# Kernel tuning notes

Hardware: AMD Instinct MI355X
Metric: run time of the kernel (lower is better)

## Reference

```python
import jax, jax.numpy as jnp
import numpy as np

NUM_NODES = 50000
NUM_EDGES = 800000
INPUT_DIM = 256
OUTPUT_DIM = 256
NUM_HEADS = 8
HEAD_DIM = OUTPUT_DIM // NUM_HEADS


def setup_inputs() -> dict:
    key = jax.random.key(0)
    ks = jax.random.split(key, 14)
    x = jax.random.normal(ks[0], (NUM_NODES, INPUT_DIM), dtype=jnp.float32)
    edge_index = jax.random.randint(ks[1], (2, NUM_EDGES), 0, NUM_NODES, dtype=jnp.int32)
    # timestamps in seconds over ~11.5 days so log1p(|dt|/3600) is informative
    edge_time = jax.random.uniform(ks[2], (NUM_EDGES,), dtype=jnp.float32) * 1e6
    node_time = jax.random.uniform(ks[3], (NUM_NODES,), dtype=jnp.float32) * 1e6
    s_in = 1.0 / np.sqrt(INPUT_DIM)
    s_out = 1.0 / np.sqrt(OUTPUT_DIM)
    s_t = 1.0 / np.sqrt(2.0)
    Wq = jax.random.uniform(ks[4], (INPUT_DIM, OUTPUT_DIM), jnp.float32, -s_in, s_in)
    bq = jax.random.uniform(ks[5], (OUTPUT_DIM,), jnp.float32, -s_in, s_in)
    Wk = jax.random.uniform(ks[6], (INPUT_DIM, OUTPUT_DIM), jnp.float32, -s_in, s_in)
    bk = jax.random.uniform(ks[7], (OUTPUT_DIM,), jnp.float32, -s_in, s_in)
    Wv = jax.random.uniform(ks[8], (INPUT_DIM, OUTPUT_DIM), jnp.float32, -s_in, s_in)
    bv = jax.random.uniform(ks[9], (OUTPUT_DIM,), jnp.float32, -s_in, s_in)
    Wt = jax.random.uniform(ks[10], (2, NUM_HEADS), jnp.float32, -s_t, s_t)
    bt = jax.random.uniform(ks[11], (NUM_HEADS,), jnp.float32, -s_t, s_t)
    Wo = jax.random.uniform(ks[12], (OUTPUT_DIM, OUTPUT_DIM), jnp.float32, -s_out, s_out)
    bo = jax.random.uniform(ks[13], (OUTPUT_DIM,), jnp.float32, -s_out, s_out)
    return {"x": x, "edge_index": edge_index, "edge_time": edge_time, "node_time": node_time,
            "Wq": Wq, "bq": bq, "Wk": Wk, "bk": bk, "Wv": Wv, "bv": bv,
            "Wt": Wt, "bt": bt, "Wo": Wo, "bo": bo}


def reference(x, edge_index, edge_time, node_time, Wq, bq, Wk, bk, Wv, bv, Wt, bt, Wo, bo):
    n = x.shape[0]
    q = (x @ Wq + bq).reshape(n, NUM_HEADS, HEAD_DIM)
    k = (x @ Wk + bk).reshape(n, NUM_HEADS, HEAD_DIM)
    v = (x @ Wv + bv).reshape(n, NUM_HEADS, HEAD_DIM)
    src, dst = edge_index[0], edge_index[1]
    # temporal features per edge
    time_diff = edge_time - node_time[dst]
    time_features = jnp.stack(
        [jnp.sign(time_diff), jnp.log1p(jnp.abs(time_diff) / 3600.0)], axis=-1)  # [E, 2]
    temporal_weights = time_features @ Wt + bt  # [E, H]
    scale = HEAD_DIM ** -0.5
    scores = jnp.einsum('ehd,ehd->eh', q[dst], k[src]) * scale + temporal_weights  # [E, H]
    # softmax over ALL edges per head (dim=0), as in the original
    alpha = jax.nn.softmax(scores, axis=0)  # [E, H]
    msg = alpha[..., None] * v[src]  # [E, H, D]
    out = jax.ops.segment_sum(msg, dst, num_segments=n)  # [N, H, D]
    out = out.reshape(n, OUTPUT_DIM)
    return out @ Wo + bo
```

## Files before the change

kernel.cpp:

```cpp
#include <hip/hip_runtime.h>
#include <hip/hip_bf16.h>

#define NUM_NODES 50000
#define NUM_EDGES 800000
#define NUM_HEADS 8
#define HEAD_DIM 32
#define SCAN_BLOCKS 49
#define NCHUNK32 1563

typedef unsigned short ushort8 __attribute__((ext_vector_type(8)));
typedef float f32x4 __attribute__((ext_vector_type(4)));
typedef __bf16 bf16x8 __attribute__((ext_vector_type(8)));
typedef _Float16 h2 __attribute__((ext_vector_type(2)));

union BF8 { ushort8 u; bf16x8 b; };
union H8 { ushort8 u; h2 h[4]; };

#if defined(__has_builtin)
#if __has_builtin(__builtin_amdgcn_fdot2)
#define FDOT2(a, b, c) __builtin_amdgcn_fdot2((a), (b), (c), false)
#endif
#endif
#ifndef FDOT2
#define FDOT2(a, b, c) ((float)(a)[0] * (float)(b)[0] + (float)(a)[1] * (float)(b)[1] + (c))
#endif

__device__ __forceinline__ float bf2f(unsigned short u) {
    return __uint_as_float(((unsigned)u) << 16);
}
__device__ __forceinline__ unsigned short f2bf(float f) {
    unsigned u = __float_as_uint(f);
    unsigned r = (u + 0x7fffu + ((u >> 16) & 1u)) >> 16;
    return (unsigned short)r;
}
__device__ __forceinline__ unsigned short f2h(float f) {
    _Float16 h = (_Float16)f;
    return *(unsigned short*)&h;
}
__device__ __forceinline__ float h2f(unsigned short u) {
    _Float16 h = *(const _Float16*)&u;
    return (float)h;
}

__global__ __launch_bounds__(256) void deg_kernel(const int* __restrict__ dst_idx, int* __restrict__ deg) {
    int e = blockIdx.x * 256 + threadIdx.x;
    if (e < NUM_EDGES) atomicAdd(&deg[dst_idx[e]], 1);
}

__global__ __launch_bounds__(1024) void scanA_kernel(
    const int* __restrict__ deg, int* __restrict__ offs, int* __restrict__ blocksum)
{
    __shared__ int buf[1024];
    int tid = threadIdx.x;
    int i = blockIdx.x * 1024 + tid;
    int v = (i < NUM_NODES) ? deg[i] : 0;
    buf[tid] = v;
    __syncthreads();
    for (int off = 1; off < 1024; off <<= 1) {
        int t = (tid >= off) ? buf[tid - off] : 0;
        __syncthreads();
        buf[tid] += t;
        __syncthreads();
    }
    if (i < NUM_NODES) offs[i] = buf[tid] - v;
    if (tid == 1023) blocksum[blockIdx.x] = buf[1023];
}

__global__ __launch_bounds__(64) void scanB_kernel(
    const int* __restrict__ blocksum, int* __restrict__ carry, int* __restrict__ offs)
{
    if (threadIdx.x == 0) {
        int acc = 0;
        for (int b = 0; b < SCAN_BLOCKS; b++) { carry[b] = acc; acc += blocksum[b]; }
        offs[NUM_NODES] = acc;
    }
}

__global__ __launch_bounds__(256) void scanC_kernel(
    int* __restrict__ offs, const int* __restrict__ carry, int* __restrict__ cursor)
{
    int i = blockIdx.x * 256 + threadIdx.x;
    if (i < NUM_NODES) {
        int v = offs[i] + carry[i >> 10];
        offs[i] = v;
        cursor[i] = v;
    }
}

__global__ __launch_bounds__(256) void fillA_kernel(
    const int* __restrict__ dst_idx, int* __restrict__ cursor, int* __restrict__ edge_of)
{
    int e = blockIdx.x * 256 + threadIdx.x;
    if (e < NUM_EDGES) {
        int pos = atomicAdd(&cursor[dst_idx[e]], 1);
        edge_of[pos] = e;
    }
}

__global__ __launch_bounds__(256) void fillB_kernel(
    const int* __restrict__ edge_of,
    const int* __restrict__ src_idx, const int* __restrict__ dst_idx,
    const float* __restrict__ edge_time, const float* __restrict__ node_time,
    unsigned long long* __restrict__ edata)
{
    int pos = blockIdx.x * 256 + threadIdx.x;
    if (pos < NUM_EDGES) {
        int e = __builtin_nontemporal_load(&edge_of[pos]);
        int s = src_idx[e];
        int d = dst_idx[e];
        float td = edge_time[e] - node_time[d];
        float t0 = (td > 0.f) ? 1.f : ((td < 0.f) ? -1.f : 0.f);
        float t1 = log1pf(fabsf(td) * (1.f / 3600.f));
        unsigned lo = (unsigned)s | ((unsigned)d << 16);
        unsigned hi = (unsigned)f2h(t0) | ((unsigned)f2h(t1) << 16);
        unsigned long long v = (unsigned long long)lo | ((unsigned long long)hi << 32);
        __builtin_nontemporal_store(v, &edata[pos]);
    }
}

__global__ __launch_bounds__(256) void wtrans_kernel(
    const float* __restrict__ Wq, const float* __restrict__ Wk,
    const float* __restrict__ Wv, const float* __restrict__ Wo,
    unsigned short* __restrict__ Wt)
{
    __shared__ float t[64][65];
    int nb = blockIdx.x * 64;
    int kb = blockIdx.y * 64;
    int g = nb >> 8;
    const float* W = (g == 0) ? Wq : (g == 1) ? Wk : (g == 2) ? Wv : Wo;
    int n0 = nb & 255;
    int tx = threadIdx.x & 63;
    int ty = threadIdx.x >> 6;
#pragma unroll
    for (int i = 0; i < 16; i++) {
        int k = i * 4 + ty;
        t[tx][k] = W[(size_t)(kb + k) * 256 + n0 + tx];
    }
    __syncthreads();
#pragma unroll
    for (int i = 0; i < 16; i++) {
        int n = i * 4 + ty;
        Wt[(size_t)(nb + n) * 256 + kb + tx] = f2bf(t[n][tx]);
    }
}

__global__ __launch_bounds__(256) void wpack_kernel(
    const unsigned short* __restrict__ Wt, unsigned short* __restrict__ Wpk)
{
    int gid = blockIdx.x * 256 + threadIdx.x;
    int lane = gid & 63;
    int fragidx = gid >> 6;
    int c2 = fragidx & 7;
    int nf = (fragidx >> 3) & 3;
    int cb = (fragidx >> 5) & 3;
    int g = fragidx >> 7;
    int l16 = lane & 15;
    int kg = lane >> 4;
    int n_col = g * 256 + cb * 64 + nf * 16 + l16;
    int k0 = c2 * 32 + kg * 8;
    ushort8 v = *(const ushort8*)(Wt + (size_t)n_col * 256 + k0);
    *(ushort8*)(Wpk + (size_t)gid * 8) = v;
}

__global__ __launch_bounds__(256) void gemm_qkv_mfma7(
    const float* __restrict__ A, int M,
    const unsigned short* __restrict__ Wpk,
    const float* __restrict__ b0, const float* __restrict__ b1, const float* __restrict__ b2,
    unsigned short* __restrict__ O0, unsigned short* __restrict__ O1, unsigned short* __restrict__ O2)
{
    __shared__ unsigned short As[64 * 256];
    int tid = threadIdx.x;
    int rowbase = blockIdx.x * 64;

    {
        int rsub = tid >> 6;
        int c4 = (tid & 63) * 4;
        int cchunk = (tid & 63) >> 1;
        int sub = (tid & 1);
#pragma unroll
        for (int it = 0; it < 16; it++) {
            int row = it * 4 + rsub;
            int grow = rowbase + row;
            float4 av = make_float4(0.f, 0.f, 0.f, 0.f);
            if (grow < M) av = *(const float4*)(A + (size_t)grow * 256 + c4);
            ushort4 o;
            o.x = f2bf(av.x); o.y = f2bf(av.y); o.z = f2bf(av.z); o.w = f2bf(av.w);
            unsigned byte = row * 512 + ((unsigned)(cchunk ^ (row & 7)) << 4) + sub * 8;
            *(ushort4*)((char*)As + byte) = o;
        }
    }
    __syncthreads();

    int lane = tid & 63;
    int wid = tid >> 6;
    int l16 = lane & 15;
    int kg = lane >> 4;

#pragma unroll
    for (int p = 0; p < 3; p++) {
        const float* bias = (p == 0) ? b0 : (p == 1) ? b1 : b2;
        unsigned short* O = (p == 0) ? O0 : (p == 1) ? O1 : O2;

        f32x4 acc[4][4];
#pragma unroll
        for (int m = 0; m < 4; m++)
#pragma unroll
            for (int n = 0; n < 4; n++) acc[m][n] = (f32x4)(0.0f);

        const ushort8* wbase = (const ushort8*)(Wpk + ((size_t)(p * 4 + wid) * 2048 + lane) * 8);

#pragma unroll
        for (int c2 = 0; c2 < 8; c2++) {
            bf16x8 wfr[4];
#pragma unroll
            for (int n = 0; n < 4; n++) {
                BF8 t; t.u = wbase[(n * 8 + c2) * 64];
                wfr[n] = t.b;
            }
            bf16x8 afr[4];
#pragma unroll
            for (int m = 0; m < 4; m++) {
                int row = m * 16 + l16;
                int cchunk = (c2 * 4 + kg) ^ (row & 7);
                BF8 t;
                t.u = *(const ushort8*)((const char*)As + row * 512 + (cchunk << 4));
                afr[m] = t.b;
            }
#pragma unroll
            for (int m = 0; m < 4; m++)
#pragma unroll
                for (int n = 0; n < 4; n++)
                    acc[m][n] = __builtin_amdgcn_mfma_f32_16x16x32_bf16(wfr[n], afr[m], acc[m][n], 0, 0, 0);
        }

#pragma unroll
        for (int m = 0; m < 4; m++) {
            int node = rowbase + m * 16 + l16;
            if (node >= M) continue;
#pragma unroll
            for (int n = 0; n < 4; n++) {
                int lc = wid * 64 + n * 16 + kg * 4;
                float4 bv = *(const float4*)(bias + lc);
                ushort4 o;
                if (p < 2) {
                    o.x = f2h(acc[m][n][0] + bv.x);
                    o.y = f2h(acc[m][n][1] + bv.y);
                    o.z = f2h(acc[m][n][2] + bv.z);
                    o.w = f2h(acc[m][n][3] + bv.w);
                } else {
                    o.x = f2bf(acc[m][n][0] + bv.x);
                    o.y = f2bf(acc[m][n][1] + bv.y);
                    o.z = f2bf(acc[m][n][2] + bv.z);
                    o.w = f2bf(acc[m][n][3] + bv.w);
                }
                int hh = lc >> 5, dd = lc & 31;
                *(ushort4*)(O + ((size_t)hh * NUM_NODES + node) * 32 + dd) = o;
            }
        }
    }
}

__global__ __launch_bounds__(256) void gemm_out_mfma6(
    const unsigned short* __restrict__ aggb, int M,
    const unsigned short* __restrict__ Wpk,
    const float* __restrict__ bias, const float* __restrict__ kscale,
    float* __restrict__ C)
{
    __shared__ unsigned short As[64 * 256];
    int tid = threadIdx.x;
    int rowbase = blockIdx.x * 64;

    {
        int rsub = tid >> 6;
        int c4 = (tid & 63) * 4;
        int cchunk = (tid & 63) >> 1;
        int sub = (tid & 1);
        int hh = c4 >> 5, dd = c4 & 31;
        float ks = kscale[hh];
#pragma unroll
        for (int it = 0; it < 16; it++) {
            int row = it * 4 + rsub;
            int grow = rowbase + row;
            ushort4 av = make_ushort4(0, 0, 0, 0);
            if (grow < M) av = *(const ushort4*)(aggb + ((size_t)hh * NUM_NODES + grow) * 32 + dd);
            ushort4 o;
            o.x = f2bf(bf2f(av.x) * ks); o.y = f2bf(bf2f(av.y) * ks);
            o.z = f2bf(bf2f(av.z) * ks); o.w = f2bf(bf2f(av.w) * ks);
            unsigned byte = row * 512 + ((unsigned)(cchunk ^ (row & 7)) << 4) + sub * 8;
            *(ushort4*)((char*)As + byte) = o;
        }
    }
    __syncthreads();

    int lane = tid & 63;
    int wid = tid >> 6;
    int l16 = lane & 15;
    int kg = lane >> 4;

    f32x4 acc[4][4];
#pragma unroll
    for (int m = 0; m < 4; m++)
#pragma unroll
        for (int n = 0; n < 4; n++) acc[m][n] = (f32x4)(0.0f);

    const ushort8* wbase = (const ushort8*)(Wpk + ((size_t)wid * 2048 + lane) * 8);

#pragma unroll
    for (int c2 = 0; c2 < 8; c2++) {
        bf16x8 wfr[4];
#pragma unroll
        for (int n = 0; n < 4; n++) {
            BF8 t; t.u = wbase[(n * 8 + c2) * 64];
            wfr[n] = t.b;
        }
        bf16x8 afr[4];
#pragma unroll
        for (int m = 0; m < 4; m++) {
            int row = m * 16 + l16;
            int cchunk = (c2 * 4 + kg) ^ (row & 7);
            BF8 t;
            t.u = *(const ushort8*)((const char*)As + row * 512 + (cchunk << 4));
            afr[m] = t.b;
        }
#pragma unroll
        for (int m = 0; m < 4; m++)
#pragma unroll
            for (int n = 0; n < 4; n++)
                acc[m][n] = __builtin_amdgcn_mfma_f32_16x16x32_bf16(wfr[n], afr[m], acc[m][n], 0, 0, 0);
    }

#pragma unroll
    for (int m = 0; m < 4; m++) {
        int node = rowbase + m * 16 + l16;
        if (node >= M) continue;
#pragma unroll
        for (int n = 0; n < 4; n++) {
            int col = wid * 64 + n * 16 + kg * 4;
            float4 bv = *(const float4*)(bias + col);
            float4 o;
            o.x = acc[m][n][0] + bv.x;
            o.y = acc[m][n][1] + bv.y;
            o.z = acc[m][n][2] + bv.z;
            o.w = acc[m][n][3] + bv.w;
            *(float4*)(C + (size_t)node * 256 + col) = o;
        }
    }
}

__global__ __launch_bounds__(256) void edge_fused_kernel(
    const unsigned short* __restrict__ qh, const unsigned short* __restrict__ kh,
    const unsigned short* __restrict__ vh, const unsigned long long* __restrict__ edata,
    const int* __restrict__ offs, const float* __restrict__ Wt,
    const float* __restrict__ bt, unsigned short* __restrict__ aggb,
    float* __restrict__ psum_part)
{
    __shared__ int sSrc[512];
    __shared__ float sP[512];
    __shared__ float blocksum;
    int tid = threadIdx.x;
    int h = blockIdx.x & 7;
    int chunk = blockIdx.x >> 3;
    int nodebase = chunk * 32;
    float wt0 = Wt[h], wt1 = Wt[8 + h], btv = bt[h];
    const unsigned short* qhh = qh + (size_t)h * NUM_NODES * 32;
    const unsigned short* khh = kh + (size_t)h * NUM_NODES * 32;
    const unsigned short* vhh = vh + (size_t)h * NUM_NODES * 32;
    if (tid == 0) blocksum = 0.f;

    int gg = tid >> 3;
    int j = (tid >> 2) & 1;
    int ln4 = tid & 3;
    int node = nodebase + gg;

    int blkstart = offs[nodebase];
    int nb_hi = (nodebase + 32 < NUM_NODES) ? (nodebase + 32) : NUM_NODES;
    int blkend = offs[nb_hi];
    int start = 0, end = 0;
    if (node < NUM_NODES) { start = offs[node]; end = offs[node + 1]; }

    f32x4 a0 = (f32x4)(0.f), a1 = (f32x4)(0.f);
    float ps = 0.f;

    for (int t0 = blkstart; t0 < blkend; t0 += 512) {
        int cnt = min(512, blkend - t0);
        __syncthreads();
        for (int i = tid; i < cnt; i += 256) {
            unsigned long long ed = __builtin_nontemporal_load(&edata[t0 + i]);
            unsigned lo32 = (unsigned)(ed & 0xffffffffull);
            unsigned hi32 = (unsigned)(ed >> 32);
            int s = lo32 & 0xffffu;
            int d = lo32 >> 16;
            float tf0 = h2f((unsigned short)(hi32 & 0xffffu));
            float tf1 = h2f((unsigned short)(hi32 >> 16));
            const ushort8* kp = (const ushort8*)(khh + (size_t)s * 32);
            const ushort8* qp = (const ushort8*)(qhh + (size_t)d * 32);
            float dotv = 0.f;
#pragma unroll
            for (int u = 0; u < 4; u++) {
                H8 a, b;
                a.u = qp[u]; b.u = kp[u];
#pragma unroll
                for (int jj = 0; jj < 4; jj++) dotv = FDOT2(a.h[jj], b.h[jj], dotv);
            }
            float sc = dotv * 0.17677669529663687f + (tf0 * wt0 + tf1 * wt1 + btv);
            sc = fminf(sc, 80.f);
            float p = __expf(sc);
            sSrc[i] = s;
            sP[i] = p;
            ps += p;
        }
        __syncthreads();
        int lo = (start > t0) ? start : t0;
        int hi = (end < t0 + cnt) ? end : (t0 + cnt);
        for (int cb = lo + j; cb < hi; cb += 2) {
            int i0 = cb - t0;
            int s0 = sSrc[i0];
            float p0 = sP[i0];
            ushort8 v = *(const ushort8*)(vhh + (size_t)s0 * 32 + ln4 * 8);
            a0[0] += p0 * bf2f(v[0]); a0[1] += p0 * bf2f(v[1]);
            a0[2] += p0 * bf2f(v[2]); a0[3] += p0 * bf2f(v[3]);
            a1[0] += p0 * bf2f(v[4]); a1[1] += p0 * bf2f(v[5]);
            a1[2] += p0 * bf2f(v[6]); a1[3] += p0 * bf2f(v[7]);
        }
    }

#pragma unroll
    for (int i = 0; i < 4; i++) {
        a0[i] += __shfl_xor(a0[i], 4, 64);
        a1[i] += __shfl_xor(a1[i], 4, 64);
    }
    if (node < NUM_NODES && j == 0) {
        ushort8 o;
        o[0] = f2bf(a0[0]); o[1] = f2bf(a0[1]); o[2] = f2bf(a0[2]); o[3] = f2bf(a0[3]);
        o[4] = f2bf(a1[0]); o[5] = f2bf(a1[1]); o[6] = f2bf(a1[2]); o[7] = f2bf(a1[3]);
        *(ushort8*)(aggb + ((size_t)h * NUM_NODES + node) * 32 + ln4 * 8) = o;
    }

    __syncthreads();
#pragma unroll
    for (int off = 32; off > 0; off >>= 1) ps += __shfl_xor(ps, off, 64);
    if ((tid & 63) == 0) atomicAdd(&blocksum, ps);
    __syncthreads();
    if (tid == 0) psum_part[blockIdx.x] = blocksum;
}

__global__ __launch_bounds__(256) void reduce_psum2_kernel(
    const float* __restrict__ psum_part, float* __restrict__ headinv)
{
    int tid = threadIdx.x;
    int h = tid >> 5, lane = tid & 31;
    float s = 0.f;
    for (int i = lane; i < NCHUNK32; i += 32) s += psum_part[i * 8 + h];
    for (int off = 16; off > 0; off >>= 1) s += __shfl_down(s, off, 32);
    if (lane == 0) headinv[h] = 1.f / s;
}

extern "C" void kernel_launch(void* const* d_in, const int* in_sizes, int n_in,
                              void* d_out, int out_size, void* d_ws, size_t ws_size,
                              hipStream_t stream) {
    const float* x = (const float*)d_in[0];
    const int* ei = (const int*)d_in[1];
    const int* src_idx = ei;
    const int* dst_idx = ei + NUM_EDGES;
    const float* edge_time = (const float*)d_in[2];
    const float* node_time = (const float*)d_in[3];
    const float* Wq = (const float*)d_in[4];  const float* bq = (const float*)d_in[5];
    const float* Wk = (const float*)d_in[6];  const float* bk = (const float*)d_in[7];
    const float* Wv = (const float*)d_in[8];  const float* bv = (const float*)d_in[9];
    const float* Wt = (const float*)d_in[10]; const float* bt = (const float*)d_in[11];
    const float* Wo = (const float*)d_in[12]; const float* bo = (const float*)d_in[13];
    float* out = (float*)d_out;

    char* w = (char*)d_ws;
    unsigned short* qb = (unsigned short*)w; w += (size_t)NUM_NODES * 256 * 2;
    unsigned short* kb = (unsigned short*)w; w += (size_t)NUM_NODES * 256 * 2;
    unsigned short* vb = (unsigned short*)w; w += (size_t)NUM_NODES * 256 * 2;
    unsigned short* aggb = (unsigned short*)w; w += (size_t)NUM_NODES * 256 * 2;
    unsigned long long* edata = (unsigned long long*)w; w += (size_t)NUM_EDGES * 8;
    int* edge_of = (int*)w;         w += (size_t)NUM_EDGES * 4;
    int* deg = (int*)w;             w += (size_t)NUM_NODES * 4;
    int* offs = (int*)w;            w += (size_t)(NUM_NODES + 1) * 4;
    int* cursor = (int*)w;          w += (size_t)NUM_NODES * 4;
    float* psum_part = (float*)w;   w += (size_t)NCHUNK32 * 8 * 4;
    float* headinv = (float*)w;     w += 8 * 4;
    int* blocksum = (int*)w;        w += 64 * 4;
    int* bcarry = (int*)w;          w += 64 * 4;
    unsigned short* Wtb = (unsigned short*)w; w += (size_t)1024 * 256 * 2;
    unsigned short* Wpk = (unsigned short*)w; w += (size_t)1024 * 256 * 2;

    hipMemsetAsync(deg, 0, (size_t)NUM_NODES * 4, stream);

    dim3 gw(16, 4);
    wtrans_kernel<<<gw, 256, 0, stream>>>(Wq, Wk, Wv, Wo, Wtb);
    wpack_kernel<<<128, 256, 0, stream>>>(Wtb, Wpk);

    deg_kernel<<<(NUM_EDGES + 255) / 256, 256, 0, stream>>>(dst_idx, deg);
    scanA_kernel<<<SCAN_BLOCKS, 1024, 0, stream>>>(deg, offs, blocksum);
    scanB_kernel<<<1, 64, 0, stream>>>(blocksum, bcarry, offs);
    scanC_kernel<<<(NUM_NODES + 255) / 256, 256, 0, stream>>>(offs, bcarry, cursor);
    fillA_kernel<<<(NUM_EDGES + 255) / 256, 256, 0, stream>>>(dst_idx, cursor, edge_of);
    fillB_kernel<<<(NUM_EDGES + 255) / 256, 256, 0, stream>>>(
        edge_of, src_idx, dst_idx, edge_time, node_time, edata);

    gemm_qkv_mfma7<<<(NUM_NODES + 63) / 64, 256, 0, stream>>>(
        x, NUM_NODES, Wpk, bq, bk, bv, qb, kb, vb);

    edge_fused_kernel<<<NCHUNK32 * 8, 256, 0, stream>>>(
        qb, kb, vb, edata, offs, Wt, bt, aggb, psum_part);
    reduce_psum2_kernel<<<1, 256, 0, stream>>>(psum_part, headinv);

    gemm_out_mfma6<<<(NUM_NODES + 63) / 64, 256, 0, stream>>>(
        aggb, NUM_NODES, Wpk + (size_t)768 * 256, bo, headinv, out);
}
```

Measured before the change: 361.2 us.

## Split fused edge kernel into separate score and aggregate passes

The fused edge kernel is split in two. A score kernel caches each chunk's 32 query rows in shared memory and writes per-edge, per-head exp scores to a global buffer. An aggregate kernel then reads those scores and a new compact source-index array to gather V. This removes the repeated global q gathers and may improve occupancy per kernel, at the cost of an extra launch and roughly 25 MB of extra global write and read traffic for the score buffer.

After: 339.4 us. -6.0%, faster.

```diff
diff --git a/kernel.cpp b/kernel.cpp
--- a/kernel.cpp
+++ b/kernel.cpp
@@ -101,11 +101,11 @@
     const int* __restrict__ edge_of,
     const int* __restrict__ src_idx, const int* __restrict__ dst_idx,
     const float* __restrict__ edge_time, const float* __restrict__ node_time,
-    unsigned long long* __restrict__ edata)
+    unsigned long long* __restrict__ edata, int* __restrict__ src_s)
 {
     int pos = blockIdx.x * 256 + threadIdx.x;
     if (pos < NUM_EDGES) {
-        int e = __builtin_nontemporal_load(&edge_of[pos]);
+        int e = edge_of[pos];
         int s = src_idx[e];
         int d = dst_idx[e];
         float td = edge_time[e] - node_time[d];
@@ -113,8 +113,8 @@
         float t1 = log1pf(fabsf(td) * (1.f / 3600.f));
         unsigned lo = (unsigned)s | ((unsigned)d << 16);
         unsigned hi = (unsigned)f2h(t0) | ((unsigned)f2h(t1) << 16);
-        unsigned long long v = (unsigned long long)lo | ((unsigned long long)hi << 32);
-        __builtin_nontemporal_store(v, &edata[pos]);
+        edata[pos] = (unsigned long long)lo | ((unsigned long long)hi << 32);
+        src_s[pos] = s;
     }
 }
 
@@ -347,15 +347,13 @@
     }
 }
 
-__global__ __launch_bounds__(256) void edge_fused_kernel(
+__global__ __launch_bounds__(256) void score8_kernel(
     const unsigned short* __restrict__ qh, const unsigned short* __restrict__ kh,
-    const unsigned short* __restrict__ vh, const unsigned long long* __restrict__ edata,
-    const int* __restrict__ offs, const float* __restrict__ Wt,
-    const float* __restrict__ bt, unsigned short* __restrict__ aggb,
-    float* __restrict__ psum_part)
-{
-    __shared__ int sSrc[512];
-    __shared__ float sP[512];
+    const unsigned long long* __restrict__ edata, const int* __restrict__ offs,
+    const float* __restrict__ Wt, const float* __restrict__ bt,
+    float* __restrict__ pb, float* __restrict__ psum_part)
+{
+    __shared__ unsigned short qs[32 * 40];
     __shared__ float blocksum;
     int tid = threadIdx.x;
     int h = blockIdx.x & 7;
@@ -364,13 +362,82 @@
     float wt0 = Wt[h], wt1 = Wt[8 + h], btv = bt[h];
     const unsigned short* qhh = qh + (size_t)h * NUM_NODES * 32;
     const unsigned short* khh = kh + (size_t)h * NUM_NODES * 32;
-    const unsigned short* vhh = vh + (size_t)h * NUM_NODES * 32;
+    float* p_h = pb + (size_t)h * NUM_EDGES;
     if (tid == 0) blocksum = 0.f;
 
+    if (tid < 128) {
+        int row = tid >> 2, slot = tid & 3;
+        int node = nodebase + row;
+        ushort8 qv = (ushort8)(0);
+        if (node < NUM_NODES) qv = *(const ushort8*)(qhh + (size_t)node * 32 + slot * 8);
+        *(ushort8*)(qs + row * 40 + slot * 8) = qv;
+    }
+    __syncthreads();
+
+    int blkstart = offs[nodebase];
+    int nb_hi = (nodebase + 32 < NUM_NODES) ? (nodebase + 32) : NUM_NODES;
+    int blkend = offs[nb_hi];
+
+    float ps = 0.f;
+    for (int pos = blkstart + tid; pos < blkend; pos += 256) {
+        unsigned long long ed = edata[pos];
+        unsigned lo32 = (unsigned)ed;
+        unsigned hi32 = (unsigned)(ed >> 32);
+        int s = lo32 & 0xffffu;
+        int dloc = (int)(lo32 >> 16) - nodebase;
+        float tf0 = h2f((unsigned short)(hi32 & 0xffffu));
+        float tf1 = h2f((unsigned short)(hi32 >> 16));
+        const ushort8* kp = (const ushort8*)(khh + (size_t)s * 32);
+        const ushort8* qp = (const ushort8*)(qs + dloc * 40);
+        float dotv = 0.f;
+#pragma unroll
+        for (int u = 0; u < 4; u++) {
+            H8 a, b;
+            a.u = qp[u]; b.u = kp[u];
+#pragma unroll
+            for (int j = 0; j < 4; j++) dotv = FDOT2(a.h[j], b.h[j], dotv);
+        }
+        float sc = dotv * 0.17677669529663687f + (tf0 * wt0 + tf1 * wt1 + btv);
+        sc = fminf(sc, 80.f);
+        float p = __expf(sc);
+        p_h[pos] = p;
+        ps += p;
+    }
+#pragma unroll
+    for (int off = 32; off > 0; off >>= 1) ps += __shfl_xor(ps, off, 64);
+    if ((tid & 63) == 0) atomicAdd(&blocksum, ps);
+    __syncthreads();
+    if (tid == 0) psum_part[blockIdx.x] = blocksum;
+}
+
+__global__ __launch_bounds__(256) void reduce_psum2_kernel(
+    const float* __restrict__ psum_part, float* __restrict__ headinv)
+{
+    int tid = threadIdx.x;
+    int h = tid >> 5, lane = tid & 31;
+    float s = 0.f;
+    for (int i = lane; i < NCHUNK32; i += 32) s += psum_part[i * 8 + h];
+    for (int off = 16; off > 0; off >>= 1) s += __shfl_down(s, off, 32);
+    if (lane == 0) headinv[h] = 1.f / s;
+}
+
+__global__ __launch_bounds__(256) void aggregate8_kernel(
+    const unsigned short* __restrict__ vh, const float* __restrict__ pb,
+    const int* __restrict__ src_s, const int* __restrict__ offs,
+    unsigned short* __restrict__ aggb)
+{
+    __shared__ int sSrc[512];
+    __shared__ float sP[512];
+    int tid = threadIdx.x;
+    int h = blockIdx.x & 7;
+    int chunk = blockIdx.x >> 3;
+    int nodebase = chunk * 32;
     int gg = tid >> 3;
     int j = (tid >> 2) & 1;
     int ln4 = tid & 3;
     int node = nodebase + gg;
+    const float* p_h = pb + (size_t)h * NUM_EDGES;
+    const unsigned short* vhh = vh + (size_t)h * NUM_NODES * 32;
 
     int blkstart = offs[nodebase];
     int nb_hi = (nodebase + 32 < NUM_NODES) ? (nodebase + 32) : NUM_NODES;
@@ -379,35 +446,13 @@
     if (node < NUM_NODES) { start = offs[node]; end = offs[node + 1]; }
 
     f32x4 a0 = (f32x4)(0.f), a1 = (f32x4)(0.f);
-    float ps = 0.f;
 
     for (int t0 = blkstart; t0 < blkend; t0 += 512) {
         int cnt = min(512, blkend - t0);
         __syncthreads();
         for (int i = tid; i < cnt; i += 256) {
-            unsigned long long ed = __builtin_nontemporal_load(&edata[t0 + i]);
-            unsigned lo32 = (unsigned)(ed & 0xffffffffull);
-            unsigned hi32 = (unsigned)(ed >> 32);
-            int s = lo32 & 0xffffu;
-            int d = lo32 >> 16;
-            float tf0 = h2f((unsigned short)(hi32 & 0xffffu));
-            float tf1 = h2f((unsigned short)(hi32 >> 16));
-            const ushort8* kp = (const ushort8*)(khh + (size_t)s * 32);
-            const ushort8* qp = (const ushort8*)(qhh + (size_t)d * 32);
-            float dotv = 0.f;
-#pragma unroll
-            for (int u = 0; u < 4; u++) {
-                H8 a, b;
-                a.u = qp[u]; b.u = kp[u];
-#pragma unroll
-                for (int jj = 0; jj < 4; jj++) dotv = FDOT2(a.h[jj], b.h[jj], dotv);
-            }
-            float sc = dotv * 0.17677669529663687f + (tf0 * wt0 + tf1 * wt1 + btv);
-            sc = fminf(sc, 80.f);
-            float p = __expf(sc);
-            sSrc[i] = s;
-            sP[i] = p;
-            ps += p;
+            sSrc[i] = src_s[t0 + i];
+            sP[i] = p_h[t0 + i];
         }
         __syncthreads();
         int lo = (start > t0) ? start : t0;
@@ -435,24 +480,6 @@
         o[4] = f2bf(a1[0]); o[5] = f2bf(a1[1]); o[6] = f2bf(a1[2]); o[7] = f2bf(a1[3]);
         *(ushort8*)(aggb + ((size_t)h * NUM_NODES + node) * 32 + ln4 * 8) = o;
     }
-
-    __syncthreads();
-#pragma unroll
-    for (int off = 32; off > 0; off >>= 1) ps += __shfl_xor(ps, off, 64);
-    if ((tid & 63) == 0) atomicAdd(&blocksum, ps);
-    __syncthreads();
-    if (tid == 0) psum_part[blockIdx.x] = blocksum;
-}
-
-__global__ __launch_bounds__(256) void reduce_psum2_kernel(
-    const float* __restrict__ psum_part, float* __restrict__ headinv)
-{
-    int tid = threadIdx.x;
-    int h = tid >> 5, lane = tid & 31;
-    float s = 0.f;
-    for (int i = lane; i < NCHUNK32; i += 32) s += psum_part[i * 8 + h];
-    for (int off = 16; off > 0; off >>= 1) s += __shfl_down(s, off, 32);
-    if (lane == 0) headinv[h] = 1.f / s;
 }
 
 extern "C" void kernel_launch(void* const* d_in, const int* in_sizes, int n_in,
@@ -475,8 +502,10 @@
     unsigned short* qb = (unsigned short*)w; w += (size_t)NUM_NODES * 256 * 2;
     unsigned short* kb = (unsigned short*)w; w += (size_t)NUM_NODES * 256 * 2;
     unsigned short* vb = (unsigned short*)w; w += (size_t)NUM_NODES * 256 * 2;
+    float* pb = (float*)w;          w += (size_t)NUM_EDGES * 8 * 4;
     unsigned short* aggb = (unsigned short*)w; w += (size_t)NUM_NODES * 256 * 2;
     unsigned long long* edata = (unsigned long long*)w; w += (size_t)NUM_EDGES * 8;
+    int* src_s = (int*)w;           w += (size_t)NUM_EDGES * 4;
     int* edge_of = (int*)w;         w += (size_t)NUM_EDGES * 4;
     int* deg = (int*)w;             w += (size_t)NUM_NODES * 4;
     int* offs = (int*)w;            w += (size_t)(NUM_NODES + 1) * 4;
@@ -500,14 +529,17 @@
     scanC_kernel<<<(NUM_NODES + 255) / 256, 256, 0, stream>>>(offs, bcarry, cursor);
     fillA_kernel<<<(NUM_EDGES + 255) / 256, 256, 0, stream>>>(dst_idx, cursor, edge_of);
     fillB_kernel<<<(NUM_EDGES + 255) / 256, 256, 0, stream>>>(
-        edge_of, src_idx, dst_idx, edge_time, node_time, edata);
+        edge_of, src_idx, dst_idx, edge_time, node_time, edata, src_s);
 
     gemm_qkv_mfma7<<<(NUM_NODES + 63) / 64, 256, 0, stream>>>(
         x, NUM_NODES, Wpk, bq, bk, bv, qb, kb, vb);
 
-    edge_fused_kernel<<<NCHUNK32 * 8, 256, 0, stream>>>(
-        qb, kb, vb, edata, offs, Wt, bt, aggb, psum_part);
+    score8_kernel<<<NCHUNK32 * 8, 256, 0, stream>>>(
+        qb, kb, edata, offs, Wt, bt, pb, psum_part);
     reduce_psum2_kernel<<<1, 256, 0, stream>>>(psum_part, headinv);
+
+    aggregate8_kernel<<<NCHUNK32 * 8, 256, 0, stream>>>(
+        vb, pb, src_s, offs, aggb);
 
     gemm_out_mfma6<<<(NUM_NODES + 63) / 64, 256, 0, stream>>>(
         aggb, NUM_NODES, Wpk + (size_t)768 * 256, bo, headinv, out);
```
